# Optimization experiments

Measured on AMD Instinct MI355X. Metric: run time of the kernel, lower is better.

The kernel has to match this reference:

```python
import jax, jax.numpy as jnp
import numpy as np

N = 50000
E = 800000
IN_DIM = 128
HID = 128
HEADS = 8
OUT_DIM = 64
LRELU_SLOPE = 0.2


def setup_inputs() -> dict:
    key = jax.random.key(0)
    ks = jax.random.split(key, 10)
    x = jax.random.normal(ks[0], (N, IN_DIM), dtype=jnp.float32)
    edge_index = jax.random.randint(ks[1], (2, E), 0, N, dtype=jnp.int64)
    c1 = HID // HEADS  # 16
    W1 = jax.random.normal(ks[2], (IN_DIM, HID), dtype=jnp.float32) * (1.0 / np.sqrt(IN_DIM))
    as1 = jax.random.normal(ks[3], (HEADS, c1), dtype=jnp.float32) * 0.1
    ad1 = jax.random.normal(ks[4], (HEADS, c1), dtype=jnp.float32) * 0.1
    b1 = jnp.zeros((HID,), dtype=jnp.float32)
    W2 = jax.random.normal(ks[5], (HID, OUT_DIM), dtype=jnp.float32) * (1.0 / np.sqrt(HID))
    as2 = jax.random.normal(ks[6], (1, OUT_DIM), dtype=jnp.float32) * 0.1
    ad2 = jax.random.normal(ks[7], (1, OUT_DIM), dtype=jnp.float32) * 0.1
    b2 = jnp.zeros((OUT_DIM,), dtype=jnp.float32)
    return {"x": x, "edge_index": edge_index, "W1": W1, "as1": as1, "ad1": ad1,
            "b1": b1, "W2": W2, "as2": as2, "ad2": ad2, "b2": b2}


def gat_conv(x, src, dst, W, a_src, a_dst, b, heads, ch, concat):
    n = x.shape[0]
    h = (x @ W).reshape(n, heads, ch)               # [N,H,C]
    alpha_s = jnp.sum(h * a_src, axis=-1)           # [N,H]
    alpha_d = jnp.sum(h * a_dst, axis=-1)           # [N,H]
    e = jax.nn.leaky_relu(alpha_s[src] + alpha_d[dst], LRELU_SLOPE)  # [E,H]
    m = jax.ops.segment_max(e, dst, num_segments=n)  # per-dst max (self-loops guarantee nonempty)
    e = jnp.exp(e - m[dst])
    denom = jax.ops.segment_sum(e, dst, num_segments=n)
    alpha = e / (denom[dst] + 1e-16)                # [E,H]
    msg = h[src] * alpha[:, :, None]                # [E,H,C]
    out = jax.ops.segment_sum(msg, dst, num_segments=n)  # [N,H,C]
    out = out.reshape(n, heads * ch) if concat else out.mean(axis=1)
    return out + b


def reference(x, edge_index, W1, as1, ad1, b1, W2, as2, ad2, b2):
    n = x.shape[0]
    loops = jnp.arange(n, dtype=edge_index.dtype)
    src = jnp.concatenate([edge_index[0], loops])   # PyG GATConv adds self-loops
    dst = jnp.concatenate([edge_index[1], loops])
    # layer 1: GATBlock (dropout is identity at eval), heads=8, concat, ELU
    h = gat_conv(x, src, dst, W1, as1, ad1, b1, HEADS, HID // HEADS, True)
    h = jax.nn.elu(h)
    # final conv: heads=1, concat=False
    out = gat_conv(h, src, dst, W2, as2, ad2, b2, 1, OUT_DIM, False)
    return jax.nn.log_softmax(out, axis=1)
```

## Files before the change

### kernel.cpp

```cpp
#include <hip/hip_runtime.h>
#include <hip/hip_bf16.h>
#include <math.h>

#define IN_DIM 128
#define HID 128
#define HEADS 8
#define OUT_DIM 64
#define SLOPE 0.2f
#define BSHIFT 7
#define BCAP 4096
#define BCAPSHIFT 12
#define EPT 8

typedef short bf16x8 __attribute__((ext_vector_type(8)));
typedef float f32x4 __attribute__((ext_vector_type(4)));

__device__ __forceinline__ float lrelu(float x) { return fmaxf(x, SLOPE * x); }
__device__ __forceinline__ float bf2f(unsigned u) { return __uint_as_float(u << 16); }
__device__ __forceinline__ unsigned short f2bf(float f) {
    unsigned u = __float_as_uint(f);
    return (unsigned short)((u + 0x7FFF + ((u >> 16) & 1)) >> 16);
}

__device__ __forceinline__ void bscatter_body(
    int blk, int* smem, const int* __restrict__ idx,
    int* __restrict__ gcursor, unsigned* __restrict__ bucket_buf,
    int E, int N, int NB) {
    int* hist  = smem;
    int* gbase = smem + 512;
    int* lbase = smem + 1024;
    int* wtot  = smem + 1536;
    int* misc  = smem + 1540;
    unsigned* sent = (unsigned*)(smem + 1552);
    unsigned* spos = (unsigned*)(smem + 3600);
    int t = threadIdx.x;
    for (int i = t; i < 512; i += 256) hist[i] = 0;
    if (t == 0) misc[1] = 0;
    __syncthreads();
    {
        int nz = (idx[2 * t + 1] != 0) + (idx[2 * t + 513] != 0);
        if (nz) atomicAdd(&misc[1], nz);
    }
    __syncthreads();
    int flag = (misc[1] > 16) ? 1 : 0;
    int e0 = blk * (256 * EPT);
    int EN = E + N;
    unsigned ent[EPT];
    int bid[EPT];
    int loc[EPT];
#pragma unroll
    for (int k = 0; k < EPT; k++) {
        int e = e0 + k * 256 + t;
        bid[k] = -1;
        if (e < EN) {
            int src, dst;
            if (e < E) {
                if (flag) { src = idx[e]; dst = idx[E + e]; }
                else      { src = idx[2 * e]; dst = idx[2 * (E + e)]; }
            } else {
                src = dst = e - E;
            }
            int b = dst >> BSHIFT;
            bid[k] = b;
            ent[k] = ((unsigned)(dst & ((1 << BSHIFT) - 1)) << 16) | (unsigned)src;
            loc[k] = atomicAdd(&hist[b], 1);
        }
    }
    __syncthreads();
    int i0 = 2 * t;
    int a = hist[i0], b2 = hist[i0 + 1];
    int ps = a + b2;
    int lane = t & 63, w = t >> 6;
    int incl = ps;
#pragma unroll
    for (int off = 1; off < 64; off <<= 1) {
        int u = __shfl_up(incl, off, 64);
        if (lane >= off) incl += u;
    }
    if (lane == 63) wtot[w] = incl;
    __syncthreads();
    int woff = 0;
    for (int k = 0; k < w; k++) woff += wtot[k];
    int ex0 = woff + incl - ps;
    lbase[i0] = ex0;
    lbase[i0 + 1] = ex0 + a;
    if (t == 255) misc[0] = woff + incl;
    for (int i = t; i < 512; i += 256) {
        int c = hist[i];
        gbase[i] = c ? atomicAdd(&gcursor[i], c) : 0;
    }
    __syncthreads();
#pragma unroll
    for (int k = 0; k < EPT; k++) {
        if (bid[k] >= 0) {
            int p = lbase[bid[k]] + loc[k];
            int pib = gbase[bid[k]] + loc[k];
            sent[p] = ent[k];
            spos[p] = (pib < BCAP) ? (((unsigned)bid[k] << BCAPSHIFT) | (unsigned)pib)
                                   : 0xFFFFFFFFu;
        }
    }
    __syncthreads();
    int tot = misc[0];
    for (int i = t; i < tot; i += 256) {
        unsigned sp = spos[i];
        if (sp != 0xFFFFFFFFu) bucket_buf[sp] = sent[i];
    }
}

__device__ __forceinline__ void gemm1_body(
    int blk, short* Wt, const float* __restrict__ x, const float* __restrict__ W1,
    unsigned short* __restrict__ h1g, int N) {
    int t = threadIdx.x;
    for (int id = t; id < 128 * 32; id += 256) {
        int k = id >> 5;
        int n0 = (id & 31) * 4;
        float4 v = *(const float4*)&W1[k * 128 + n0];
        Wt[(n0 + 0) * 136 + k] = (short)f2bf(v.x);
        Wt[(n0 + 1) * 136 + k] = (short)f2bf(v.y);
        Wt[(n0 + 2) * 136 + k] = (short)f2bf(v.z);
        Wt[(n0 + 3) * 136 + k] = (short)f2bf(v.w);
    }
    __syncthreads();
    int wv = t >> 6, lane = t & 63;
    int m = lane & 15, q = lane >> 4;
    int row = blk * 64 + wv * 16 + m;
    f32x4 acc[8];
#pragma unroll
    for (int j = 0; j < 8; j++) acc[j] = (f32x4){0.f, 0.f, 0.f, 0.f};
#pragma unroll
    for (int k0 = 0; k0 < 128; k0 += 32) {
        bf16x8 a = {0, 0, 0, 0, 0, 0, 0, 0};
        if (row < N) {
            const float* xp = &x[(size_t)row * 128 + k0 + q * 8];
            float4 u0 = *(const float4*)xp;
            float4 u1 = *(const float4*)(xp + 4);
            a[0] = (short)f2bf(u0.x); a[1] = (short)f2bf(u0.y);
            a[2] = (short)f2bf(u0.z); a[3] = (short)f2bf(u0.w);
            a[4] = (short)f2bf(u1.x); a[5] = (short)f2bf(u1.y);
            a[6] = (short)f2bf(u1.z); a[7] = (short)f2bf(u1.w);
        }
#pragma unroll
        for (int j = 0; j < 8; j++) {
            bf16x8 b = *(const bf16x8*)&Wt[(j * 16 + m) * 136 + k0 + q * 8];
            acc[j] = __builtin_amdgcn_mfma_f32_16x16x32_bf16(a, b, acc[j], 0, 0, 0);
        }
    }
    int rbase = blk * 64 + wv * 16 + q * 4;
#pragma unroll
    for (int r = 0; r < 4; r++) {
        int rr = rbase + r;
        if (rr < N) {
#pragma unroll
            for (int j = 0; j < 8; j++)
                h1g[(size_t)rr * 128 + j * 16 + m] = f2bf(acc[j][r]);
        }
    }
}

__global__ __launch_bounds__(256) void k1_kernel(
    const int* __restrict__ idx, int* __restrict__ gcursor,
    unsigned* __restrict__ bucket_buf,
    const float* __restrict__ x, const float* __restrict__ W1,
    unsigned short* __restrict__ h1g, int E, int N, int NB, int GS) {
    __shared__ long long smem[4352];
    if ((int)blockIdx.x < GS)
        bscatter_body(blockIdx.x, (int*)smem, idx, gcursor, bucket_buf, E, N, NB);
    else
        gemm1_body(blockIdx.x - GS, (short*)smem, x, W1, h1g, N);
}

__device__ __forceinline__ void bsort_body(
    int b, const int* __restrict__ gcursor, const unsigned* __restrict__ bucket_buf,
    int* __restrict__ row_start, int* __restrict__ sorted_src, int N, int NB) {
    __shared__ int cnt[128];
    __shared__ int cur[128];
    __shared__ int red[4];
    __shared__ int s_w0;
    __shared__ int srt[BCAP];
    int t = threadIdx.x;
    if (t < 128) cnt[t] = 0;
    int partial = 0;
    for (int i = t; i < b; i += 256) partial += min(gcursor[i], BCAP);
#pragma unroll
    for (int msk = 32; msk > 0; msk >>= 1) partial += __shfl_xor(partial, msk, 64);
    if ((t & 63) == 0) red[t >> 6] = partial;
    __syncthreads();
    int bbase = red[0] + red[1] + red[2] + red[3];
    int c = min(gcursor[b], BCAP);
    const unsigned* buf = bucket_buf + ((size_t)b << BCAPSHIFT);
    for (int i = t; i < c; i += 256)
        atomicAdd(&cnt[(buf[i] >> 16) & 127], 1);
    __syncthreads();
    int v = (t < 128) ? cnt[t] : 0;
    int lane = t & 63;
    int incl = v;
#pragma unroll
    for (int off = 1; off < 64; off <<= 1) {
        int u = __shfl_up(incl, off, 64);
        if (lane >= off) incl += u;
    }
    if (t == 63) s_w0 = incl;
    __syncthreads();
    if (t < 128) {
        int excl = incl - v + ((t >= 64) ? s_w0 : 0);
        cur[t] = excl;
        int node = (b << BSHIFT) + t;
        if (node <= N) row_start[node] = bbase + excl;
    }
    __syncthreads();
    for (int i = t; i < c; i += 256) {
        unsigned e = buf[i];
        int lp = atomicAdd(&cur[(e >> 16) & 127], 1);
        srt[lp] = (int)(e & 0xFFFFu);
    }
    __syncthreads();
    for (int i = t; i < c; i += 256)
        sorted_src[bbase + i] = srt[i];
}

__device__ __forceinline__ void alpha1_body(
    int blk, const unsigned short* __restrict__ h1g,
    const float* __restrict__ a_s, const float* __restrict__ a_d,
    float* __restrict__ as_n, float* __restrict__ ad_n, int N) {
    int gid = blk * 256 + threadIdx.x;
    if (gid >= N * 8) return;
    int n = gid >> 3, hd = gid & 7;
    const uint4* hp = (const uint4*)(h1g + (size_t)n * 128 + hd * 16);
    uint4 u0 = hp[0], u1 = hp[1];
    unsigned uu[8] = {u0.x, u0.y, u0.z, u0.w, u1.x, u1.y, u1.z, u1.w};
    const float* sp = a_s + hd * 16;
    const float* dp = a_d + hd * 16;
    float s = 0.f, d = 0.f;
#pragma unroll
    for (int k = 0; k < 8; k++) {
        float lo = bf2f(uu[k] & 0xffffu), hi = bf2f(uu[k] >> 16);
        s += lo * sp[2 * k] + hi * sp[2 * k + 1];
        d += lo * dp[2 * k] + hi * dp[2 * k + 1];
    }
    as_n[gid] = s;
    ad_n[gid] = d;
}

__global__ __launch_bounds__(256) void k2_kernel(
    const int* __restrict__ gcursor, const unsigned* __restrict__ bucket_buf,
    int* __restrict__ row_start, int* __restrict__ sorted_src,
    const unsigned short* __restrict__ h1g,
    const float* __restrict__ a_s, const float* __restrict__ a_d,
    float* __restrict__ as_n, float* __restrict__ ad_n, int N, int NB, int EN) {
    if (blockIdx.x == 0 && threadIdx.x < 16) sorted_src[EN + threadIdx.x] = 0;
    if ((int)blockIdx.x < NB)
        bsort_body(blockIdx.x, gcursor, bucket_buf, row_start, sorted_src, N, NB);
    else
        alpha1_body(blockIdx.x - NB, h1g, a_s, a_d, as_n, ad_n, N);
}

__global__ __launch_bounds__(256) void agg1_kernel(
    const int* __restrict__ row_start, const int* __restrict__ sorted_src,
    const float* __restrict__ as_n, const float* __restrict__ ad_n,
    const unsigned short* __restrict__ h1g, const float* __restrict__ b1,
    unsigned short* __restrict__ h1act, int N) {
    int node = blockIdx.x * 4 + (threadIdx.x >> 6);
    int lane = threadIdx.x & 63;
    if (node >= N) return;
    int slot = lane >> 4, cg = lane & 15;
    int e8 = lane >> 3, hd8 = lane & 7;
    int wl_a = (slot << 3) | (cg >> 1);
    int wl_b = ((slot + 4) << 3) | (cg >> 1);
    float ad_w = ad_n[node * 8 + hd8];
    int beg = row_start[node], end = row_start[node + 1];
    float acc[8];
#pragma unroll
    for (int k = 0; k < 8; k++) acc[k] = 0.f;
    float denom = 0.f;
    for (int i = beg; i < end; i += 16) {
        int se1 = sorted_src[i + e8];
        int se2 = sorted_src[i + 8 + e8];
        float w1 = __expf(lrelu(as_n[se1 * 8 + hd8] + ad_w));
        float w2 = __expf(lrelu(as_n[se2 * 8 + hd8] + ad_w));
        w1 = (i + e8 < end) ? w1 : 0.f;
        w2 = (i + 8 + e8 < end) ? w2 : 0.f;
        float wva = __shfl(w1, wl_a, 64);
        float wvb = __shfl(w1, wl_b, 64);
        float wvc = __shfl(w2, wl_a, 64);
        float wvd = __shfl(w2, wl_b, 64);
        int sga = __shfl(se1, wl_a, 64);
        int sgb = __shfl(se1, wl_b, 64);
        int sgc = __shfl(se2, wl_a, 64);
        int sgd = __shfl(se2, wl_b, 64);
        uint4 hva = *(const uint4*)&h1g[(size_t)sga * 128 + cg * 8];
        uint4 hvb = *(const uint4*)&h1g[(size_t)sgb * 128 + cg * 8];
        uint4 hvc = *(const uint4*)&h1g[(size_t)sgc * 128 + cg * 8];
        uint4 hvd = *(const uint4*)&h1g[(size_t)sgd * 128 + cg * 8];
        acc[0] += wva * bf2f(hva.x & 0xffffu) + wvb * bf2f(hvb.x & 0xffffu)
                + wvc * bf2f(hvc.x & 0xffffu) + wvd * bf2f(hvd.x & 0xffffu);
        acc[1] += wva * bf2f(hva.x >> 16) + wvb * bf2f(hvb.x >> 16)
                + wvc * bf2f(hvc.x >> 16) + wvd * bf2f(hvd.x >> 16);
        acc[2] += wva * bf2f(hva.y & 0xffffu) + wvb * bf2f(hvb.y & 0xffffu)
                + wvc * bf2f(hvc.y & 0xffffu) + wvd * bf2f(hvd.y & 0xffffu);
        acc[3] += wva * bf2f(hva.y >> 16) + wvb * bf2f(hvb.y >> 16)
                + wvc * bf2f(hvc.y >> 16) + wvd * bf2f(hvd.y >> 16);
        acc[4] += wva * bf2f(hva.z & 0xffffu) + wvb * bf2f(hvb.z & 0xffffu)
                + wvc * bf2f(hvc.z & 0xffffu) + wvd * bf2f(hvd.z & 0xffffu);
        acc[5] += wva * bf2f(hva.z >> 16) + wvb * bf2f(hvb.z >> 16)
                + wvc * bf2f(hvc.z >> 16) + wvd * bf2f(hvd.z >> 16);
        acc[6] += wva * bf2f(hva.w & 0xffffu) + wvb * bf2f(hvb.w & 0xffffu)
                + wvc * bf2f(hvc.w & 0xffffu) + wvd * bf2f(hvd.w & 0xffffu);
        acc[7] += wva * bf2f(hva.w >> 16) + wvb * bf2f(hvb.w >> 16)
                + wvc * bf2f(hvc.w >> 16) + wvd * bf2f(hvd.w >> 16);
        denom += wva + wvb + wvc + wvd;
    }
#pragma unroll
    for (int msk = 16; msk < 64; msk <<= 1) {
#pragma unroll
        for (int k = 0; k < 8; k++) acc[k] += __shfl_xor(acc[k], msk, 64);
        denom += __shfl_xor(denom, msk, 64);
    }
    if (slot == 0) {
        float inv = 1.f / (denom + 1e-16f);
        int c0 = cg * 8;
        unsigned ow[4];
#pragma unroll
        for (int p = 0; p < 4; p++) {
            float v0 = acc[2 * p] * inv + b1[c0 + 2 * p];
            float v1 = acc[2 * p + 1] * inv + b1[c0 + 2 * p + 1];
            v0 = (v0 > 0.f) ? v0 : (__expf(v0) - 1.f);
            v1 = (v1 > 0.f) ? v1 : (__expf(v1) - 1.f);
            ow[p] = (unsigned)f2bf(v0) | ((unsigned)f2bf(v1) << 16);
        }
        *(uint4*)&h1act[(size_t)node * 128 + c0] = make_uint4(ow[0], ow[1], ow[2], ow[3]);
    }
}

__global__ __launch_bounds__(256) void gemm2_kernel(
    const unsigned short* __restrict__ h1act, const float* __restrict__ W2,
    const float* __restrict__ a_s, const float* __restrict__ a_d,
    unsigned short* __restrict__ h2g, float* __restrict__ as_n,
    float* __restrict__ ad_n, int N) {
    __shared__ short Wt[64 * 136];
    int t = threadIdx.x;
    for (int id = t; id < 128 * 16; id += 256) {
        int k = id >> 4;
        int n0 = (id & 15) * 4;
        float4 v = *(const float4*)&W2[k * 64 + n0];
        Wt[(n0 + 0) * 136 + k] = (short)f2bf(v.x);
        Wt[(n0 + 1) * 136 + k] = (short)f2bf(v.y);
        Wt[(n0 + 2) * 136 + k] = (short)f2bf(v.z);
        Wt[(n0 + 3) * 136 + k] = (short)f2bf(v.w);
    }
    __syncthreads();
    int wv = t >> 6, lane = t & 63;
    int m = lane & 15, q = lane >> 4;
    int row = blockIdx.x * 64 + wv * 16 + m;
    f32x4 acc[4];
#pragma unroll
    for (int j = 0; j < 4; j++) acc[j] = (f32x4){0.f, 0.f, 0.f, 0.f};
#pragma unroll
    for (int k0 = 0; k0 < 128; k0 += 32) {
        bf16x8 a = {0, 0, 0, 0, 0, 0, 0, 0};
        if (row < N) a = *(const bf16x8*)&h1act[(size_t)row * 128 + k0 + q * 8];
#pragma unroll
        for (int j = 0; j < 4; j++) {
            bf16x8 b = *(const bf16x8*)&Wt[(j * 16 + m) * 136 + k0 + q * 8];
            acc[j] = __builtin_amdgcn_mfma_f32_16x16x32_bf16(a, b, acc[j], 0, 0, 0);
        }
    }
    float asl[4], adl[4];
#pragma unroll
    for (int j = 0; j < 4; j++) { asl[j] = a_s[j * 16 + m]; adl[j] = a_d[j * 16 + m]; }
    int rbase = blockIdx.x * 64 + wv * 16 + q * 4;
#pragma unroll
    for (int r = 0; r < 4; r++) {
        int rr = rbase + r;
        float s = 0.f, d = 0.f;
#pragma unroll
        for (int j = 0; j < 4; j++) {
            s += acc[j][r] * asl[j];
            d += acc[j][r] * adl[j];
        }
#pragma unroll
        for (int msk = 8; msk > 0; msk >>= 1) {
            s += __shfl_xor(s, msk, 64);
            d += __shfl_xor(d, msk, 64);
        }
        if (rr < N) {
            if (m == 0) { as_n[rr] = s; ad_n[rr] = d; }
#pragma unroll
            for (int j = 0; j < 4; j++)
                h2g[(size_t)rr * 64 + j * 16 + m] = f2bf(acc[j][r]);
        }
    }
}

__global__ __launch_bounds__(256) void agg2_kernel(
    const int* __restrict__ row_start, const int* __restrict__ sorted_src,
    const float* __restrict__ as_n, const float* __restrict__ ad_n,
    const unsigned short* __restrict__ h2g, const float* __restrict__ b2,
    float* __restrict__ out, int N) {
    int node = blockIdx.x * 4 + (threadIdx.x >> 6);
    int lane = threadIdx.x & 63;
    if (node >= N) return;
    int slot = lane >> 4, cg = lane & 15;
    int e8 = lane & 7;
    float adv = ad_n[node];
    int beg = row_start[node], end = row_start[node + 1];
    float acc[4];
#pragma unroll
    for (int k = 0; k < 4; k++) acc[k] = 0.f;
    float denom = 0.f;
    for (int i = beg; i < end; i += 16) {
        int se1 = sorted_src[i + e8];
        int se2 = sorted_src[i + 8 + e8];
        float w1 = __expf(lrelu(as_n[se1] + adv));
        float w2 = __expf(lrelu(as_n[se2] + adv));
        w1 = (i + e8 < end) ? w1 : 0.f;
        w2 = (i + 8 + e8 < end) ? w2 : 0.f;
        float wva = __shfl(w1, slot, 64);
        float wvb = __shfl(w1, slot + 4, 64);
        float wvc = __shfl(w2, slot, 64);
        float wvd = __shfl(w2, slot + 4, 64);
        int sga = __shfl(se1, slot, 64);
        int sgb = __shfl(se1, slot + 4, 64);
        int sgc = __shfl(se2, slot, 64);
        int sgd = __shfl(se2, slot + 4, 64);
        uint2 hva = *(const uint2*)&h2g[(size_t)sga * 64 + cg * 4];
        uint2 hvb = *(const uint2*)&h2g[(size_t)sgb * 64 + cg * 4];
        uint2 hvc = *(const uint2*)&h2g[(size_t)sgc * 64 + cg * 4];
        uint2 hvd = *(const uint2*)&h2g[(size_t)sgd * 64 + cg * 4];
        acc[0] += wva * bf2f(hva.x & 0xffffu) + wvb * bf2f(hvb.x & 0xffffu)
                + wvc * bf2f(hvc.x & 0xffffu) + wvd * bf2f(hvd.x & 0xffffu);
        acc[1] += wva * bf2f(hva.x >> 16) + wvb * bf2f(hvb.x >> 16)
                + wvc * bf2f(hvc.x >> 16) + wvd * bf2f(hvd.x >> 16);
        acc[2] += wva * bf2f(hva.y & 0xffffu) + wvb * bf2f(hvb.y & 0xffffu)
                + wvc * bf2f(hvc.y & 0xffffu) + wvd * bf2f(hvd.y & 0xffffu);
        acc[3] += wva * bf2f(hva.y >> 16) + wvb * bf2f(hvb.y >> 16)
                + wvc * bf2f(hvc.y >> 16) + wvd * bf2f(hvd.y >> 16);
        denom += wva + wvb + wvc + wvd;
    }
#pragma unroll
    for (int msk = 16; msk < 64; msk <<= 1) {
#pragma unroll
        for (int k = 0; k < 4; k++) acc[k] += __shfl_xor(acc[k], msk, 64);
        denom += __shfl_xor(denom, msk, 64);
    }
    if (slot == 0) {
        float inv = 1.f / (denom + 1e-16f);
        int c0 = cg * 4;
        float v[4];
#pragma unroll
        for (int k = 0; k < 4; k++) v[k] = acc[k] * inv + b2[c0 + k];
        float m = fmaxf(fmaxf(v[0], v[1]), fmaxf(v[2], v[3]));
#pragma unroll
        for (int msk = 8; msk > 0; msk >>= 1) m = fmaxf(m, __shfl_xor(m, msk, 64));
        float ex = __expf(v[0] - m) + __expf(v[1] - m) + __expf(v[2] - m) + __expf(v[3] - m);
#pragma unroll
        for (int msk = 8; msk > 0; msk >>= 1) ex += __shfl_xor(ex, msk, 64);
        float lse = m + __logf(ex);
        float4 ov = make_float4(v[0] - lse, v[1] - lse, v[2] - lse, v[3] - lse);
        *(float4*)&out[(size_t)node * 64 + c0] = ov;
    }
}

extern "C" void kernel_launch(void* const* d_in, const int* in_sizes, int n_in,
                              void* d_out, int out_size, void* d_ws, size_t ws_size,
                              hipStream_t stream) {
    const float* x   = (const float*)d_in[0];
    const int*   idx = (const int*)d_in[1];
    const float* W1  = (const float*)d_in[2];
    const float* as1 = (const float*)d_in[3];
    const float* ad1 = (const float*)d_in[4];
    const float* b1  = (const float*)d_in[5];
    const float* W2  = (const float*)d_in[6];
    const float* as2 = (const float*)d_in[7];
    const float* ad2 = (const float*)d_in[8];
    const float* b2  = (const float*)d_in[9];
    float* out = (float*)d_out;

    const int N = in_sizes[0] / IN_DIM;
    const int E = in_sizes[1] / 2;
    const int EN = E + N;
    const int NB = (N + (1 << BSHIFT) - 1) >> BSHIFT;
    const int GS = (EN + 256 * EPT - 1) / (256 * EPT);
    const int A1 = (N * 8 + 255) / 256;
    const int T1 = (N + 63) / 64;

    unsigned short* h1g   = (unsigned short*)d_ws;
    unsigned short* h1act = h1g + (size_t)N * 128;
    unsigned short* h2g   = h1act + (size_t)N * 128;
    float* as1n = (float*)(h2g + (size_t)N * 64);
    float* ad1n = as1n + (size_t)N * 8;
    float* as2n = ad1n + (size_t)N * 8;
    float* ad2n = as2n + (size_t)N;
    int* row_start  = (int*)(ad2n + (size_t)N);
    int* gcursor    = row_start + N + 1;
    unsigned* bucket_buf = (unsigned*)(gcursor + 512);
    int* sorted_src = (int*)(bucket_buf + ((size_t)NB << BCAPSHIFT));
    (void)ws_size; (void)n_in; (void)out_size;

    hipMemsetAsync(gcursor, 0, 512 * sizeof(int), stream);

    k1_kernel<<<GS + T1, 256, 0, stream>>>(idx, gcursor, bucket_buf,
                                           x, W1, h1g, E, N, NB, GS);
    k2_kernel<<<NB + A1, 256, 0, stream>>>(gcursor, bucket_buf, row_start, sorted_src,
                                           h1g, as1, ad1, as1n, ad1n, N, NB, EN);
    agg1_kernel<<<(N + 3) / 4, 256, 0, stream>>>(row_start, sorted_src, as1n, ad1n, h1g, b1, h1act, N);
    gemm2_kernel<<<T1, 256, 0, stream>>>(h1act, W2, as2, ad2, h2g, as2n, ad2n, N);
    agg2_kernel<<<(N + 3) / 4, 256, 0, stream>>>(row_start, sorted_src, as2n, ad2n, h2g, b2, out, N);
}
```

Baseline: 213.8 us.

## Fuse attention logits into GEMM1 epilogue and use quarter-wave per node aggregation

Computes the per-head source and destination attention logits in the first GEMM's epilogue through cross-lane reductions on the MFMA accumulators, so the separate alpha pass no longer re-reads h1. Both aggregation kernels now give each node 16 lanes instead of a full wave, processing 4 edges per step, which drops the cross-slot reduction and the idle-lane epilogue. This raises per-lane serial work and the number of gather iterations per node, and the logits now come from fp32 accumulators rather than the bf16-rounded features.

```diff
diff --git a/kernel.cpp b/kernel.cpp
--- a/kernel.cpp
+++ b/kernel.cpp
@@ -110,7 +110,9 @@
 
 __device__ __forceinline__ void gemm1_body(
     int blk, short* Wt, const float* __restrict__ x, const float* __restrict__ W1,
-    unsigned short* __restrict__ h1g, int N) {
+    const float* __restrict__ a_s, const float* __restrict__ a_d,
+    unsigned short* __restrict__ h1g, float* __restrict__ as_n,
+    float* __restrict__ ad_n, int N) {
     int t = threadIdx.x;
     for (int id = t; id < 128 * 32; id += 256) {
         int k = id >> 5;
@@ -146,11 +148,34 @@
             acc[j] = __builtin_amdgcn_mfma_f32_16x16x32_bf16(a, b, acc[j], 0, 0, 0);
         }
     }
+    float asl[8], adl[8];
+#pragma unroll
+    for (int j = 0; j < 8; j++) { asl[j] = a_s[j * 16 + m]; adl[j] = a_d[j * 16 + m]; }
     int rbase = blk * 64 + wv * 16 + q * 4;
 #pragma unroll
     for (int r = 0; r < 4; r++) {
         int rr = rbase + r;
+        float sv[8], dv[8];
+#pragma unroll
+        for (int j = 0; j < 8; j++) {
+            sv[j] = acc[j][r] * asl[j];
+            dv[j] = acc[j][r] * adl[j];
+        }
+#pragma unroll
+        for (int msk = 1; msk < 16; msk <<= 1) {
+#pragma unroll
+            for (int j = 0; j < 8; j++) {
+                sv[j] += __shfl_xor(sv[j], msk, 64);
+                dv[j] += __shfl_xor(dv[j], msk, 64);
+            }
+        }
         if (rr < N) {
+            if (m == 0) {
+                *(float4*)&as_n[(size_t)rr * 8]     = make_float4(sv[0], sv[1], sv[2], sv[3]);
+                *(float4*)&as_n[(size_t)rr * 8 + 4] = make_float4(sv[4], sv[5], sv[6], sv[7]);
+                *(float4*)&ad_n[(size_t)rr * 8]     = make_float4(dv[0], dv[1], dv[2], dv[3]);
+                *(float4*)&ad_n[(size_t)rr * 8 + 4] = make_float4(dv[4], dv[5], dv[6], dv[7]);
+            }
 #pragma unroll
             for (int j = 0; j < 8; j++)
                 h1g[(size_t)rr * 128 + j * 16 + m] = f2bf(acc[j][r]);
@@ -162,12 +187,14 @@
     const int* __restrict__ idx, int* __restrict__ gcursor,
     unsigned* __restrict__ bucket_buf,
     const float* __restrict__ x, const float* __restrict__ W1,
-    unsigned short* __restrict__ h1g, int E, int N, int NB, int GS) {
+    const float* __restrict__ a_s, const float* __restrict__ a_d,
+    unsigned short* __restrict__ h1g, float* __restrict__ as_n,
+    float* __restrict__ ad_n, int E, int N, int NB, int GS) {
     __shared__ long long smem[4352];
     if ((int)blockIdx.x < GS)
         bscatter_body(blockIdx.x, (int*)smem, idx, gcursor, bucket_buf, E, N, NB);
     else
-        gemm1_body(blockIdx.x - GS, (short*)smem, x, W1, h1g, N);
+        gemm1_body(blockIdx.x - GS, (short*)smem, x, W1, a_s, a_d, h1g, as_n, ad_n, N);
 }
 
 __device__ __forceinline__ void bsort_body(
@@ -219,40 +246,12 @@
         sorted_src[bbase + i] = srt[i];
 }
 
-__device__ __forceinline__ void alpha1_body(
-    int blk, const unsigned short* __restrict__ h1g,
-    const float* __restrict__ a_s, const float* __restrict__ a_d,
-    float* __restrict__ as_n, float* __restrict__ ad_n, int N) {
-    int gid = blk * 256 + threadIdx.x;
-    if (gid >= N * 8) return;
-    int n = gid >> 3, hd = gid & 7;
-    const uint4* hp = (const uint4*)(h1g + (size_t)n * 128 + hd * 16);
-    uint4 u0 = hp[0], u1 = hp[1];
-    unsigned uu[8] = {u0.x, u0.y, u0.z, u0.w, u1.x, u1.y, u1.z, u1.w};
-    const float* sp = a_s + hd * 16;
-    const float* dp = a_d + hd * 16;
-    float s = 0.f, d = 0.f;
-#pragma unroll
-    for (int k = 0; k < 8; k++) {
-        float lo = bf2f(uu[k] & 0xffffu), hi = bf2f(uu[k] >> 16);
-        s += lo * sp[2 * k] + hi * sp[2 * k + 1];
-        d += lo * dp[2 * k] + hi * dp[2 * k + 1];
-    }
-    as_n[gid] = s;
-    ad_n[gid] = d;
-}
-
 __global__ __launch_bounds__(256) void k2_kernel(
     const int* __restrict__ gcursor, const unsigned* __restrict__ bucket_buf,
     int* __restrict__ row_start, int* __restrict__ sorted_src,
-    const unsigned short* __restrict__ h1g,
-    const float* __restrict__ a_s, const float* __restrict__ a_d,
-    float* __restrict__ as_n, float* __restrict__ ad_n, int N, int NB, int EN) {
+    int N, int NB, int EN) {
     if (blockIdx.x == 0 && threadIdx.x < 16) sorted_src[EN + threadIdx.x] = 0;
-    if ((int)blockIdx.x < NB)
-        bsort_body(blockIdx.x, gcursor, bucket_buf, row_start, sorted_src, N, NB);
-    else
-        alpha1_body(blockIdx.x - NB, h1g, a_s, a_d, as_n, ad_n, N);
+    bsort_body(blockIdx.x, gcursor, bucket_buf, row_start, sorted_src, N, NB);
 }
 
 __global__ __launch_bounds__(256) void agg1_kernel(
@@ -260,76 +259,60 @@
     const float* __restrict__ as_n, const float* __restrict__ ad_n,
     const unsigned short* __restrict__ h1g, const float* __restrict__ b1,
     unsigned short* __restrict__ h1act, int N) {
-    int node = blockIdx.x * 4 + (threadIdx.x >> 6);
     int lane = threadIdx.x & 63;
+    int g = lane >> 4, j = lane & 15;
+    int node = blockIdx.x * 16 + (threadIdx.x >> 6) * 4 + g;
     if (node >= N) return;
-    int slot = lane >> 4, cg = lane & 15;
-    int e8 = lane >> 3, hd8 = lane & 7;
-    int wl_a = (slot << 3) | (cg >> 1);
-    int wl_b = ((slot + 4) << 3) | (cg >> 1);
-    float ad_w = ad_n[node * 8 + hd8];
+    int e4 = j >> 2;
+    int hh = (j & 3) * 2;
+    int hd = j >> 1;
+    int hsel = hd & 1;
+    int wsrc = hd >> 1;
+    float2 adp = *(const float2*)&ad_n[(size_t)node * 8 + hh];
     int beg = row_start[node], end = row_start[node + 1];
     float acc[8];
 #pragma unroll
     for (int k = 0; k < 8; k++) acc[k] = 0.f;
     float denom = 0.f;
-    for (int i = beg; i < end; i += 16) {
-        int se1 = sorted_src[i + e8];
-        int se2 = sorted_src[i + 8 + e8];
-        float w1 = __expf(lrelu(as_n[se1 * 8 + hd8] + ad_w));
-        float w2 = __expf(lrelu(as_n[se2 * 8 + hd8] + ad_w));
-        w1 = (i + e8 < end) ? w1 : 0.f;
-        w2 = (i + 8 + e8 < end) ? w2 : 0.f;
-        float wva = __shfl(w1, wl_a, 64);
-        float wvb = __shfl(w1, wl_b, 64);
-        float wvc = __shfl(w2, wl_a, 64);
-        float wvd = __shfl(w2, wl_b, 64);
-        int sga = __shfl(se1, wl_a, 64);
-        int sgb = __shfl(se1, wl_b, 64);
-        int sgc = __shfl(se2, wl_a, 64);
-        int sgd = __shfl(se2, wl_b, 64);
-        uint4 hva = *(const uint4*)&h1g[(size_t)sga * 128 + cg * 8];
-        uint4 hvb = *(const uint4*)&h1g[(size_t)sgb * 128 + cg * 8];
-        uint4 hvc = *(const uint4*)&h1g[(size_t)sgc * 128 + cg * 8];
-        uint4 hvd = *(const uint4*)&h1g[(size_t)sgd * 128 + cg * 8];
-        acc[0] += wva * bf2f(hva.x & 0xffffu) + wvb * bf2f(hvb.x & 0xffffu)
-                + wvc * bf2f(hvc.x & 0xffffu) + wvd * bf2f(hvd.x & 0xffffu);
-        acc[1] += wva * bf2f(hva.x >> 16) + wvb * bf2f(hvb.x >> 16)
-                + wvc * bf2f(hvc.x >> 16) + wvd * bf2f(hvd.x >> 16);
-        acc[2] += wva * bf2f(hva.y & 0xffffu) + wvb * bf2f(hvb.y & 0xffffu)
-                + wvc * bf2f(hvc.y & 0xffffu) + wvd * bf2f(hvd.y & 0xffffu);
-        acc[3] += wva * bf2f(hva.y >> 16) + wvb * bf2f(hvb.y >> 16)
-                + wvc * bf2f(hvc.y >> 16) + wvd * bf2f(hvd.y >> 16);
-        acc[4] += wva * bf2f(hva.z & 0xffffu) + wvb * bf2f(hvb.z & 0xffffu)
-                + wvc * bf2f(hvc.z & 0xffffu) + wvd * bf2f(hvd.z & 0xffffu);
-        acc[5] += wva * bf2f(hva.z >> 16) + wvb * bf2f(hvb.z >> 16)
-                + wvc * bf2f(hvc.z >> 16) + wvd * bf2f(hvd.z >> 16);
-        acc[6] += wva * bf2f(hva.w & 0xffffu) + wvb * bf2f(hvb.w & 0xffffu)
-                + wvc * bf2f(hvc.w & 0xffffu) + wvd * bf2f(hvd.w & 0xffffu);
-        acc[7] += wva * bf2f(hva.w >> 16) + wvb * bf2f(hvb.w >> 16)
-                + wvc * bf2f(hvc.w >> 16) + wvd * bf2f(hvd.w >> 16);
-        denom += wva + wvb + wvc + wvd;
-    }
-#pragma unroll
-    for (int msk = 16; msk < 64; msk <<= 1) {
-#pragma unroll
-        for (int k = 0; k < 8; k++) acc[k] += __shfl_xor(acc[k], msk, 64);
-        denom += __shfl_xor(denom, msk, 64);
-    }
-    if (slot == 0) {
-        float inv = 1.f / (denom + 1e-16f);
-        int c0 = cg * 8;
-        unsigned ow[4];
-#pragma unroll
-        for (int p = 0; p < 4; p++) {
-            float v0 = acc[2 * p] * inv + b1[c0 + 2 * p];
-            float v1 = acc[2 * p + 1] * inv + b1[c0 + 2 * p + 1];
-            v0 = (v0 > 0.f) ? v0 : (__expf(v0) - 1.f);
-            v1 = (v1 > 0.f) ? v1 : (__expf(v1) - 1.f);
-            ow[p] = (unsigned)f2bf(v0) | ((unsigned)f2bf(v1) << 16);
-        }
-        *(uint4*)&h1act[(size_t)node * 128 + c0] = make_uint4(ow[0], ow[1], ow[2], ow[3]);
-    }
+    for (int i = beg; i < end; i += 4) {
+        int se = sorted_src[i + e4];
+        float2 asp = *(const float2*)&as_n[(size_t)se * 8 + hh];
+        float w0 = __expf(lrelu(asp.x + adp.x));
+        float w1 = __expf(lrelu(asp.y + adp.y));
+        bool val = (i + e4 < end);
+        w0 = val ? w0 : 0.f;
+        w1 = val ? w1 : 0.f;
+#pragma unroll
+        for (int e = 0; e < 4; e++) {
+            int sl = e * 4 + wsrc;
+            int sg = __shfl(se, sl, 16);
+            float wa = __shfl(w0, sl, 16);
+            float wb = __shfl(w1, sl, 16);
+            float wv = hsel ? wb : wa;
+            uint4 hv = *(const uint4*)&h1g[(size_t)sg * 128 + j * 8];
+            acc[0] += wv * bf2f(hv.x & 0xffffu);
+            acc[1] += wv * bf2f(hv.x >> 16);
+            acc[2] += wv * bf2f(hv.y & 0xffffu);
+            acc[3] += wv * bf2f(hv.y >> 16);
+            acc[4] += wv * bf2f(hv.z & 0xffffu);
+            acc[5] += wv * bf2f(hv.z >> 16);
+            acc[6] += wv * bf2f(hv.w & 0xffffu);
+            acc[7] += wv * bf2f(hv.w >> 16);
+            denom += wv;
+        }
+    }
+    float inv = 1.f / (denom + 1e-16f);
+    int c0 = j * 8;
+    unsigned ow[4];
+#pragma unroll
+    for (int p = 0; p < 4; p++) {
+        float v0 = acc[2 * p] * inv + b1[c0 + 2 * p];
+        float v1 = acc[2 * p + 1] * inv + b1[c0 + 2 * p + 1];
+        v0 = (v0 > 0.f) ? v0 : (__expf(v0) - 1.f);
+        v1 = (v1 > 0.f) ? v1 : (__expf(v1) - 1.f);
+        ow[p] = (unsigned)f2bf(v0) | ((unsigned)f2bf(v1) << 16);
+    }
+    *(uint4*)&h1act[(size_t)node * 128 + c0] = make_uint4(ow[0], ow[1], ow[2], ow[3]);
 }
 
 __global__ __launch_bounds__(256) void gemm2_kernel(
@@ -397,68 +380,46 @@
     const float* __restrict__ as_n, const float* __restrict__ ad_n,
     const unsigned short* __restrict__ h2g, const float* __restrict__ b2,
     float* __restrict__ out, int N) {
-    int node = blockIdx.x * 4 + (threadIdx.x >> 6);
     int lane = threadIdx.x & 63;
+    int g = lane >> 4, j = lane & 15;
+    int node = blockIdx.x * 16 + (threadIdx.x >> 6) * 4 + g;
     if (node >= N) return;
-    int slot = lane >> 4, cg = lane & 15;
-    int e8 = lane & 7;
+    int e4 = j >> 2;
     float adv = ad_n[node];
     int beg = row_start[node], end = row_start[node + 1];
     float acc[4];
 #pragma unroll
     for (int k = 0; k < 4; k++) acc[k] = 0.f;
     float denom = 0.f;
-    for (int i = beg; i < end; i += 16) {
-        int se1 = sorted_src[i + e8];
-        int se2 = sorted_src[i + 8 + e8];
-        float w1 = __expf(lrelu(as_n[se1] + adv));
-        float w2 = __expf(lrelu(as_n[se2] + adv));
-        w1 = (i + e8 < end) ? w1 : 0.f;
-        w2 = (i + 8 + e8 < end) ? w2 : 0.f;
-        float wva = __shfl(w1, slot, 64);
-        float wvb = __shfl(w1, slot + 4, 64);
-        float wvc = __shfl(w2, slot, 64);
-        float wvd = __shfl(w2, slot + 4, 64);
-        int sga = __shfl(se1, slot, 64);
-        int sgb = __shfl(se1, slot + 4, 64);
-        int sgc = __shfl(se2, slot, 64);
-        int sgd = __shfl(se2, slot + 4, 64);
-        uint2 hva = *(const uint2*)&h2g[(size_t)sga * 64 + cg * 4];
-        uint2 hvb = *(const uint2*)&h2g[(size_t)sgb * 64 + cg * 4];
-        uint2 hvc = *(const uint2*)&h2g[(size_t)sgc * 64 + cg * 4];
-        uint2 hvd = *(const uint2*)&h2g[(size_t)sgd * 64 + cg * 4];
-        acc[0] += wva * bf2f(hva.x & 0xffffu) + wvb * bf2f(hvb.x & 0xffffu)
-                + wvc * bf2f(hvc.x & 0xffffu) + wvd * bf2f(hvd.x & 0xffffu);
-        acc[1] += wva * bf2f(hva.x >> 16) + wvb * bf2f(hvb.x >> 16)
-                + wvc * bf2f(hvc.x >> 16) + wvd * bf2f(hvd.x >> 16);
-        acc[2] += wva * bf2f(hva.y & 0xffffu) + wvb * bf2f(hvb.y & 0xffffu)
-                + wvc * bf2f(hvc.y & 0xffffu) + wvd * bf2f(hvd.y & 0xffffu);
-        acc[3] += wva * bf2f(hva.y >> 16) + wvb * bf2f(hvb.y >> 16)
-                + wvc * bf2f(hvc.y >> 16) + wvd * bf2f(hvd.y >> 16);
-        denom += wva + wvb + wvc + wvd;
-    }
-#pragma unroll
-    for (int msk = 16; msk < 64; msk <<= 1) {
-#pragma unroll
-        for (int k = 0; k < 4; k++) acc[k] += __shfl_xor(acc[k], msk, 64);
-        denom += __shfl_xor(denom, msk, 64);
-    }
-    if (slot == 0) {
-        float inv = 1.f / (denom + 1e-16f);
-        int c0 = cg * 4;
-        float v[4];
-#pragma unroll
-        for (int k = 0; k < 4; k++) v[k] = acc[k] * inv + b2[c0 + k];
-        float m = fmaxf(fmaxf(v[0], v[1]), fmaxf(v[2], v[3]));
-#pragma unroll
-        for (int msk = 8; msk > 0; msk >>= 1) m = fmaxf(m, __shfl_xor(m, msk, 64));
-        float ex = __expf(v[0] - m) + __expf(v[1] - m) + __expf(v[2] - m) + __expf(v[3] - m);
-#pragma unroll
-        for (int msk = 8; msk > 0; msk >>= 1) ex += __shfl_xor(ex, msk, 64);
-        float lse = m + __logf(ex);
-        float4 ov = make_float4(v[0] - lse, v[1] - lse, v[2] - lse, v[3] - lse);
-        *(float4*)&out[(size_t)node * 64 + c0] = ov;
-    }
+    for (int i = beg; i < end; i += 4) {
+        int se = sorted_src[i + e4];
+        float w = __expf(lrelu(as_n[se] + adv));
+        w = (i + e4 < end) ? w : 0.f;
+#pragma unroll
+        for (int e = 0; e < 4; e++) {
+            int sg = __shfl(se, e * 4, 16);
+            float wvv = __shfl(w, e * 4, 16);
+            uint2 hv = *(const uint2*)&h2g[(size_t)sg * 64 + j * 4];
+            acc[0] += wvv * bf2f(hv.x & 0xffffu);
+            acc[1] += wvv * bf2f(hv.x >> 16);
+            acc[2] += wvv * bf2f(hv.y & 0xffffu);
+            acc[3] += wvv * bf2f(hv.y >> 16);
+            denom += wvv;
+        }
+    }
+    float inv = 1.f / (denom + 1e-16f);
+    int c0 = j * 4;
+    float v[4];
+#pragma unroll
+    for (int k = 0; k < 4; k++) v[k] = acc[k] * inv + b2[c0 + k];
+    float mx = fmaxf(fmaxf(v[0], v[1]), fmaxf(v[2], v[3]));
+#pragma unroll
+    for (int msk = 8; msk > 0; msk >>= 1) mx = fmaxf(mx, __shfl_xor(mx, msk, 64));
+    float ex = __expf(v[0] - mx) + __expf(v[1] - mx) + __expf(v[2] - mx) + __expf(v[3] - mx);
+#pragma unroll
+    for (int msk = 8; msk > 0; msk >>= 1) ex += __shfl_xor(ex, msk, 64);
+    float lse = mx + __logf(ex);
+    *(float4*)&out[(size_t)node * 64 + c0] = make_float4(v[0] - lse, v[1] - lse, v[2] - lse, v[3] - lse);
 }
 
 extern "C" void kernel_launch(void* const* d_in, const int* in_sizes, int n_in,
@@ -481,7 +442,6 @@
     const int EN = E + N;
     const int NB = (N + (1 << BSHIFT) - 1) >> BSHIFT;
     const int GS = (EN + 256 * EPT - 1) / (256 * EPT);
-    const int A1 = (N * 8 + 255) / 256;
     const int T1 = (N + 63) / 64;
 
     unsigned short* h1g   = (unsigned short*)d_ws;
@@ -500,10 +460,9 @@
     hipMemsetAsync(gcursor, 0, 512 * sizeof(int), stream);
 
     k1_kernel<<<GS + T1, 256, 0, stream>>>(idx, gcursor, bucket_buf,
-                                           x, W1, h1g, E, N, NB, GS);
-    k2_kernel<<<NB + A1, 256, 0, stream>>>(gcursor, bucket_buf, row_start, sorted_src,
-                                           h1g, as1, ad1, as1n, ad1n, N, NB, EN);
-    agg1_kernel<<<(N + 3) / 4, 256, 0, stream>>>(row_start, sorted_src, as1n, ad1n, h1g, b1, h1act, N);
+                                           x, W1, as1, ad1, h1g, as1n, ad1n, E, N, NB, GS);
+    k2_kernel<<<NB, 256, 0, stream>>>(gcursor, bucket_buf, row_start, sorted_src, N, NB, EN);
+    agg1_kernel<<<(N + 15) / 16, 256, 0, stream>>>(row_start, sorted_src, as1n, ad1n, h1g, b1, h1act, N);
     gemm2_kernel<<<T1, 256, 0, stream>>>(h1act, W2, as2, ad2, h2g, as2n, ad2n, N);
-    agg2_kernel<<<(N + 3) / 4, 256, 0, stream>>>(row_start, sorted_src, as2n, ad2n, h2g, b2, out, N);
-}
+    agg2_kernel<<<(N + 15) / 16, 256, 0, stream>>>(row_start, sorted_src, as2n, ad2n, h2g, b2, out, N);
+}
```

Measured after the change: 211.6 us. About the same (-1.0%).
